# Performance work log

Measured on AMD Instinct MI355X. Metric: run time of the kernel, lower is better.

## Reference

```python
import jax, jax.numpy as jnp
import numpy as np

NUM_PARTS = 10
COS_W = 10.0
COS_K = 100.0
EPS = 1e-6

B, V, F, VHD = 512, 6890, 13776, 20000


def setup_inputs() -> dict:
    key = jax.random.key(0)
    k1, k2, k3, k4, k5 = jax.random.split(key, 5)
    vertices = jax.random.normal(k1, (B, V, 3), dtype=jnp.float32)
    bary = jax.random.uniform(k2, (VHD, 3), dtype=jnp.float32)
    faces = jax.random.randint(k3, (F, 3), 0, V)
    hd_fid = jax.random.randint(k4, (VHD,), 0, F)
    part_fid = jax.random.randint(k5, (F,), 0, NUM_PARTS)
    return {"vertices": vertices, "bary": bary, "faces": faces,
            "hd_fid": hd_fid, "part_fid": part_fid}


def reference(vertices, bary, faces, hd_fid, part_fid):
    # --- per-part mesh volume (signed tetra volumes, segment-summed by part) ---
    tri = vertices[:, faces]                       # [B, F, 3, 3] gather face corners
    t0, t1, t2 = tri[:, :, 0], tri[:, :, 1], tri[:, :, 2]
    vol_f = jnp.einsum('bfi,bfi->bf', jnp.cross(t0, t1), t2) / 6.0   # [B, F]
    fid_onehot = jax.nn.one_hot(part_fid, NUM_PARTS, dtype=vertices.dtype)  # [F, P]
    per_part_volume = vol_f @ fid_onehot           # [B, P]

    # --- HDfy: barycentric sampling of HD vertices on faces ---
    w = bary / jnp.sum(bary, axis=-1, keepdims=True)          # barycentric weights [VHD,3]
    vidx = faces[hd_fid]                                       # [VHD, 3]
    hd_corners = vertices[:, vidx]                             # [B, VHD, 3, 3]
    vertices_hd = jnp.einsum('bvkd,vk->bvd', hd_corners, w)    # [B, VHD, 3]

    # --- per-HD-vertex part volume (bmm with one-hot == gather) ---
    hd_part = part_fid[hd_fid]                                 # [VHD]
    vol_hd = per_part_volume[:, hd_part]                       # [B, VHD]

    # --- center of mass ---
    com = jnp.sum(vertices_hd * vol_hd[..., None], axis=1) / jnp.sum(vol_hd, axis=1, keepdims=True)  # [B,3]

    # --- center of pressure via height-based pressure weights ---
    h = vertices_hd[:, :, 1]                                   # [B, VHD], ground plane at y=0
    inside = (h < 0.0).astype(vertices_hd.dtype)
    outside = (h >= 0.0).astype(vertices_hd.dtype)
    pw = inside * (1.0 - COS_K * h) + outside * jnp.exp(-COS_W * h)
    cop = jnp.sum(vertices_hd * pw[..., None], axis=1) / (jnp.sum(pw, axis=1, keepdims=True) + EPS)  # [B,3]

    # --- stability loss: xz distance between COM and COP ---
    d = com - cop
    return jnp.sqrt(d[:, 0] ** 2 + d[:, 2] ** 2)               # [B]
```

## Files before the change

### kernel.cpp

```cpp
#include <hip/hip_runtime.h>
#include <math.h>

#define NB     512
#define NV     6890
#define NF     13776
#define NVHD   20000
#define NPARTS 10
#define NTHREADS 1024
#define NWAVES (NTHREADS/64)
#define CUT    6697
#define NCHF   ((NF + 63) / 64)
#define NCHH   ((NVHD + 63) / 64)
#define FBLK   ((NF + 255) / 256)
#define HBLK   ((NVHD + 255) / 256)

__global__ __launch_bounds__(256) void count_kernel(
    const int* __restrict__ faces, const int* __restrict__ part_fid,
    const int* __restrict__ hd_fid,
    int* __restrict__ cntF,
    int* __restrict__ cntH)
{
    const int wv = threadIdx.x >> 6, lane = threadIdx.x & 63;
    if (blockIdx.x < FBLK) {
        int c = blockIdx.x * 4 + wv;
        int i = c * 64 + lane;
        int key = -1;
        if (i < NF) {
            int i0 = faces[3*i+0], i1 = faces[3*i+1], i2 = faces[3*i+2];
            bool bad = (i0 >= CUT) || (i1 >= CUT) || (i2 >= CUT);
            key = bad ? 10 : part_fid[i];
        }
        #pragma unroll
        for (int q = 0; q < 11; q++) {
            unsigned long long m = __ballot(key == q);
            if (lane == 0) cntF[q * NCHF + c] = (int)__popcll(m);
        }
    } else {
        int c = (blockIdx.x - FBLK) * 4 + wv;
        if (c < NCHH) {
            int i = c * 64 + lane;
            int key = -1;
            if (i < NVHD) {
                int fid = hd_fid[i];
                int i0 = faces[3*fid+0], i1 = faces[3*fid+1], i2 = faces[3*fid+2];
                key = ((i0 >= CUT) || (i1 >= CUT) || (i2 >= CUT)) ? 1 : 0;
            }
            #pragma unroll
            for (int q = 0; q < 2; q++) {
                unsigned long long m = __ballot(key == q);
                if (lane == 0) cntH[q * NCHH + c] = (int)__popcll(m);
            }
        }
    }
}

__global__ __launch_bounds__(1024) void scan_kernel(
    int* __restrict__ cntF, int* __restrict__ cntH, int* __restrict__ offs)
{
    __shared__ int rowtot[13];
    const int wv = threadIdx.x >> 6, lane = threadIdx.x & 63;
    if (wv < 11) {
        int* row = cntF + wv * NCHF;
        int carry = 0;
        #pragma unroll
        for (int seg = 0; seg < (NCHF + 63) / 64; seg++) {
            int idx = seg * 64 + lane;
            int v = (idx < NCHF) ? row[idx] : 0;
            int incl = v;
            #pragma unroll
            for (int off = 1; off < 64; off <<= 1) { int n = __shfl_up(incl, off, 64); if (lane >= off) incl += n; }
            if (idx < NCHF) row[idx] = incl - v + carry;
            carry += __shfl(incl, 63, 64);
        }
        if (lane == 0) rowtot[wv] = carry;
    } else if (wv < 13) {
        int r = wv - 11;
        int* row = cntH + r * NCHH;
        int carry = 0;
        #pragma unroll
        for (int seg = 0; seg < (NCHH + 63) / 64; seg++) {
            int idx = seg * 64 + lane;
            int v = (idx < NCHH) ? row[idx] : 0;
            int incl = v;
            #pragma unroll
            for (int off = 1; off < 64; off <<= 1) { int n = __shfl_up(incl, off, 64); if (lane >= off) incl += n; }
            if (idx < NCHH) row[idx] = incl - v + carry;
            carry += __shfl(incl, 63, 64);
        }
        if (lane == 0) rowtot[11 + r] = carry;
    }
    __syncthreads();
    if (threadIdx.x == 0) {
        int r = 0;
        #pragma unroll
        for (int q = 0; q < 11; q++) { offs[q] = r; r += rowtot[q]; }
        offs[11] = r;
        offs[12] = 0;
        offs[13] = rowtot[11];
        offs[14] = rowtot[11] + rowtot[12];
    }
}

__global__ __launch_bounds__(256) void scatter_kernel(
    const float* __restrict__ bary, const int* __restrict__ faces,
    const int* __restrict__ hd_fid, const int* __restrict__ part_fid,
    const int* __restrict__ cntF, const int* __restrict__ cntH,
    const int* __restrict__ offs,
    uint2* __restrict__ f_sorted, uint4* __restrict__ hd_sorted)
{
    const int wv = threadIdx.x >> 6, lane = threadIdx.x & 63;
    const unsigned long long low = (1ull << lane) - 1ull;
    if (blockIdx.x < FBLK) {
        int c = blockIdx.x * 4 + wv;
        int i = c * 64 + lane;
        int key = -1; uint2 ft = make_uint2(0u, 0u);
        if (i < NF) {
            int i0 = faces[3*i+0], i1 = faces[3*i+1], i2 = faces[3*i+2];
            int p  = part_fid[i];
            bool bad = (i0 >= CUT) || (i1 >= CUT) || (i2 >= CUT);
            key = bad ? 10 : p;
            ft = make_uint2((unsigned)i0 | ((unsigned)i1 << 16),
                            (unsigned)i2 | ((unsigned)p  << 16));
        }
        #pragma unroll
        for (int q = 0; q < 11; q++) {
            unsigned long long m = __ballot(key == q);
            if (key == q) {
                int rank = (int)__popcll(m & low);
                f_sorted[offs[q] + cntF[q * NCHF + c] + rank] = ft;
            }
        }
    } else {
        int c = (blockIdx.x - FBLK) * 4 + wv;
        if (c < NCHH) {
            int i = c * 64 + lane;
            int key = -1; uint4 hp = make_uint4(0u, 0u, 0u, 0u);
            if (i < NVHD) {
                int fid = hd_fid[i];
                int i0 = faces[3*fid+0], i1 = faces[3*fid+1], i2 = faces[3*fid+2];
                float b0 = bary[3*i+0], b1 = bary[3*i+1], b2 = bary[3*i+2];
                float inv = 1.0f / (b0 + b1 + b2);
                hp = make_uint4((unsigned)i0 | ((unsigned)i1 << 16),
                                (unsigned)i2 | ((unsigned)part_fid[fid] << 16),
                                __float_as_uint(b0*inv), __float_as_uint(b1*inv));
                key = ((i0 >= CUT) || (i1 >= CUT) || (i2 >= CUT)) ? 1 : 0;
            }
            #pragma unroll
            for (int q = 0; q < 2; q++) {
                unsigned long long m = __ballot(key == q);
                if (key == q) {
                    int rank = (int)__popcll(m & low);
                    hd_sorted[offs[12 + q] + cntH[q * NCHH + c] + rank] = hp;
                }
            }
        }
    }
}

__global__ __launch_bounds__(NTHREADS, 8) void stab_kernel(
    const float* __restrict__ vertices,
    const uint2* __restrict__ f_sorted,
    const uint4* __restrict__ hd_sorted,
    const int*   __restrict__ offs,
    float*       __restrict__ out)
{
    __shared__ float2 sxy[CUT];
    __shared__ float  szz[CUT];
    __shared__ float  spart[NPARTS];
    __shared__ float  sredp[NWAVES][NPARTS];

    const int tid  = threadIdx.x;
    const int b    = blockIdx.x;
    const int wave = tid >> 6;
    const int lane = tid & 63;
    const float* __restrict__ vb = vertices + (size_t)b * (NV * 3);

    int offF[12];
    #pragma unroll
    for (int q = 0; q < 12; q++) offF[q] = offs[q];
    const int hClean = offs[13];

    for (int v = tid; v < CUT; v += NTHREADS) {
        float x = vb[3 * v + 0];
        float y = vb[3 * v + 1];
        float z = vb[3 * v + 2];
        sxy[v] = make_float2(x, y);
        szz[v] = z;
    }
    __syncthreads();

    float accp[NPARTS];
    #pragma unroll
    for (int q = 0; q < NPARTS; q++) accp[q] = 0.f;

    #pragma unroll
    for (int p = 0; p < NPARTS; p++) {
        float va = 0.f;
        for (int f = offF[p] + tid; f < offF[p + 1]; f += NTHREADS) {
            uint2 ft = f_sorted[f];
            int i0 = ft.x & 0xFFFF, i1 = ft.x >> 16, i2 = ft.y & 0xFFFF;
            float2 t0 = sxy[i0]; float z0 = szz[i0];
            float2 t1 = sxy[i1]; float z1 = szz[i1];
            float2 t2 = sxy[i2]; float z2 = szz[i2];
            float cx = t0.y * z1   - z0   * t1.y;
            float cy = z0   * t1.x - t0.x * z1;
            float cz = t0.x * t1.y - t0.y * t1.x;
            va += (cx * t2.x + cy * t2.y + cz * z2) * (1.0f / 6.0f);
        }
        accp[p] += va;
    }
    for (int f = offF[10] + tid; f < NF; f += NTHREADS) {
        uint2 ft = f_sorted[f];
        int i0 = ft.x & 0xFFFF, i1 = ft.x >> 16;
        int i2 = ft.y & 0xFFFF, p  = (int)(ft.y >> 16);
        float x0 = vb[3*i0+0], y0 = vb[3*i0+1], z0 = vb[3*i0+2];
        float x1 = vb[3*i1+0], y1 = vb[3*i1+1], z1 = vb[3*i1+2];
        float x2 = vb[3*i2+0], y2 = vb[3*i2+1], z2 = vb[3*i2+2];
        float cx = y0 * z1 - z0 * y1;
        float cy = z0 * x1 - x0 * z1;
        float cz = x0 * y1 - y0 * x1;
        float vol = (cx * x2 + cy * y2 + cz * z2) * (1.0f / 6.0f);
        #pragma unroll
        for (int q = 0; q < NPARTS; q++) accp[q] += (p == q) ? vol : 0.f;
    }

    #pragma unroll
    for (int q = 0; q < NPARTS; q++) {
        float s = accp[q];
        #pragma unroll
        for (int off = 32; off > 0; off >>= 1) s += __shfl_down(s, off, 64);
        accp[q] = s;
    }
    if (lane == 0) {
        #pragma unroll
        for (int q = 0; q < NPARTS; q++) sredp[wave][q] = accp[q];
    }
    __syncthreads();
    if (tid < NPARTS) {
        float s = 0.f;
        #pragma unroll
        for (int w = 0; w < NWAVES; w++) s += sredp[w][tid];
        spart[tid] = s;
    }
    __syncthreads();

    float sVx = 0.f, sVz = 0.f, sVol = 0.f;
    float sPx = 0.f, sPz = 0.f, sPw = 0.f;

    #pragma unroll 2
    for (int v = tid; v < hClean; v += NTHREADS) {
        uint4 hp = hd_sorted[v];
        int i0 = hp.x & 0xFFFF, i1 = hp.x >> 16;
        int i2 = hp.y & 0xFFFF, p  = (int)(hp.y >> 16);
        float w0 = __uint_as_float(hp.z);
        float w1 = __uint_as_float(hp.w);
        float w2 = 1.0f - w0 - w1;
        float2 t0 = sxy[i0]; float z0 = szz[i0];
        float2 t1 = sxy[i1]; float z1 = szz[i1];
        float2 t2 = sxy[i2]; float z2 = szz[i2];
        float x = w0 * t0.x + w1 * t1.x + w2 * t2.x;
        float y = w0 * t0.y + w1 * t1.y + w2 * t2.y;
        float z = w0 * z0   + w1 * z1   + w2 * z2;
        float vol = spart[p];
        float pw  = (y < 0.f) ? fmaf(-100.f, y, 1.f) : __expf(-10.f * y);
        sVx += x * vol;  sVz += z * vol;  sVol += vol;
        sPx += x * pw;   sPz += z * pw;   sPw += pw;
    }
    for (int v = hClean + tid; v < NVHD; v += NTHREADS) {
        uint4 hp = hd_sorted[v];
        int i0 = hp.x & 0xFFFF, i1 = hp.x >> 16;
        int i2 = hp.y & 0xFFFF, p  = (int)(hp.y >> 16);
        float w0 = __uint_as_float(hp.z);
        float w1 = __uint_as_float(hp.w);
        float w2 = 1.0f - w0 - w1;
        float x0 = vb[3*i0+0], y0 = vb[3*i0+1], z0 = vb[3*i0+2];
        float x1 = vb[3*i1+0], y1 = vb[3*i1+1], z1 = vb[3*i1+2];
        float x2 = vb[3*i2+0], y2 = vb[3*i2+1], z2 = vb[3*i2+2];
        float x = w0 * x0 + w1 * x1 + w2 * x2;
        float y = w0 * y0 + w1 * y1 + w2 * y2;
        float z = w0 * z0 + w1 * z1 + w2 * z2;
        float vol = spart[p];
        float pw  = (y < 0.f) ? fmaf(-100.f, y, 1.f) : __expf(-10.f * y);
        sVx += x * vol;  sVz += z * vol;  sVol += vol;
        sPx += x * pw;   sPz += z * pw;   sPw += pw;
    }

    float vals[6] = {sVx, sVz, sVol, sPx, sPz, sPw};
    #pragma unroll
    for (int q = 0; q < 6; q++) {
        float s = vals[q];
        #pragma unroll
        for (int off = 32; off > 0; off >>= 1) s += __shfl_down(s, off, 64);
        vals[q] = s;
    }
    float* sred6 = &sredp[0][0];
    if (lane == 0) {
        #pragma unroll
        for (int q = 0; q < 6; q++) sred6[wave * 6 + q] = vals[q];
    }
    __syncthreads();
    if (tid == 0) {
        float r[6];
        #pragma unroll
        for (int q = 0; q < 6; q++) {
            float s = 0.f;
            #pragma unroll
            for (int w = 0; w < NWAVES; w++) s += sred6[w * 6 + q];
            r[q] = s;
        }
        float invVol = 1.0f / r[2];
        float invPw  = 1.0f / (r[5] + 1e-6f);
        float comx = r[0] * invVol, comz = r[1] * invVol;
        float copx = r[3] * invPw,  copz = r[4] * invPw;
        float d0 = comx - copx, d2 = comz - copz;
        out[b] = sqrtf(d0 * d0 + d2 * d2);
    }
}

extern "C" void kernel_launch(void* const* d_in, const int* in_sizes, int n_in,
                              void* d_out, int out_size, void* d_ws, size_t ws_size,
                              hipStream_t stream) {
    const float* vertices = (const float*)d_in[0];
    const float* bary     = (const float*)d_in[1];
    const int*   faces    = (const int*)d_in[2];
    const int*   hd_fid   = (const int*)d_in[3];
    const int*   part_fid = (const int*)d_in[4];
    float* out = (float*)d_out;

    char* ws = (char*)d_ws;
    uint4* hd_sorted = (uint4*)ws;
    uint2* f_sorted  = (uint2*)(ws + 320000);
    int*   cntF      = (int*)(ws + 320000 + 110208);
    int*   cntH      = (int*)(ws + 320000 + 110208 + 9504);
    int*   offs      = (int*)(ws + 320000 + 110208 + 9504 + 2504);

    count_kernel<<<FBLK + HBLK, 256, 0, stream>>>(faces, part_fid, hd_fid, cntF, cntH);
    scan_kernel<<<1, 1024, 0, stream>>>(cntF, cntH, offs);
    scatter_kernel<<<FBLK + HBLK, 256, 0, stream>>>(bary, faces, hd_fid, part_fid,
                                                    cntF, cntH, offs, f_sorted, hd_sorted);
    stab_kernel<<<NB, NTHREADS, 0, stream>>>(vertices, f_sorted, hd_sorted, offs, out);
}
```

Baseline: 54.83 us.

## Bucket HD vertices by part to factor volume weights out of inner loop

```diff
diff --git a/kernel.cpp b/kernel.cpp
--- a/kernel.cpp
+++ b/kernel.cpp
@@ -13,6 +13,7 @@
 #define NCHH   ((NVHD + 63) / 64)
 #define FBLK   ((NF + 255) / 256)
 #define HBLK   ((NVHD + 255) / 256)
+#define NOFFS  33
 
 __global__ __launch_bounds__(256) void count_kernel(
     const int* __restrict__ faces, const int* __restrict__ part_fid,
@@ -43,10 +44,12 @@
             if (i < NVHD) {
                 int fid = hd_fid[i];
                 int i0 = faces[3*fid+0], i1 = faces[3*fid+1], i2 = faces[3*fid+2];
-                key = ((i0 >= CUT) || (i1 >= CUT) || (i2 >= CUT)) ? 1 : 0;
+                int p  = part_fid[fid];
+                bool bad = (i0 >= CUT) || (i1 >= CUT) || (i2 >= CUT);
+                key = bad ? (10 + p) : p;
             }
             #pragma unroll
-            for (int q = 0; q < 2; q++) {
+            for (int q = 0; q < 20; q++) {
                 unsigned long long m = __ballot(key == q);
                 if (lane == 0) cntH[q * NCHH + c] = (int)__popcll(m);
             }
@@ -57,37 +60,22 @@
 __global__ __launch_bounds__(1024) void scan_kernel(
     int* __restrict__ cntF, int* __restrict__ cntH, int* __restrict__ offs)
 {
-    __shared__ int rowtot[13];
+    __shared__ int rowtot[31];
     const int wv = threadIdx.x >> 6, lane = threadIdx.x & 63;
-    if (wv < 11) {
-        int* row = cntF + wv * NCHF;
+    for (int r = wv; r < 31; r += NWAVES) {
+        int  len = (r < 11) ? NCHF : NCHH;
+        int* row = (r < 11) ? (cntF + r * NCHF) : (cntH + (r - 11) * NCHH);
         int carry = 0;
-        #pragma unroll
-        for (int seg = 0; seg < (NCHF + 63) / 64; seg++) {
+        for (int seg = 0; seg < (len + 63) / 64; seg++) {
             int idx = seg * 64 + lane;
-            int v = (idx < NCHF) ? row[idx] : 0;
+            int v = (idx < len) ? row[idx] : 0;
             int incl = v;
             #pragma unroll
             for (int off = 1; off < 64; off <<= 1) { int n = __shfl_up(incl, off, 64); if (lane >= off) incl += n; }
-            if (idx < NCHF) row[idx] = incl - v + carry;
+            if (idx < len) row[idx] = incl - v + carry;
             carry += __shfl(incl, 63, 64);
         }
-        if (lane == 0) rowtot[wv] = carry;
-    } else if (wv < 13) {
-        int r = wv - 11;
-        int* row = cntH + r * NCHH;
-        int carry = 0;
-        #pragma unroll
-        for (int seg = 0; seg < (NCHH + 63) / 64; seg++) {
-            int idx = seg * 64 + lane;
-            int v = (idx < NCHH) ? row[idx] : 0;
-            int incl = v;
-            #pragma unroll
-            for (int off = 1; off < 64; off <<= 1) { int n = __shfl_up(incl, off, 64); if (lane >= off) incl += n; }
-            if (idx < NCHH) row[idx] = incl - v + carry;
-            carry += __shfl(incl, 63, 64);
-        }
-        if (lane == 0) rowtot[11 + r] = carry;
+        if (lane == 0) rowtot[r] = carry;
     }
     __syncthreads();
     if (threadIdx.x == 0) {
@@ -95,9 +83,10 @@
         #pragma unroll
         for (int q = 0; q < 11; q++) { offs[q] = r; r += rowtot[q]; }
         offs[11] = r;
-        offs[12] = 0;
-        offs[13] = rowtot[11];
-        offs[14] = rowtot[11] + rowtot[12];
+        r = 0;
+        #pragma unroll
+        for (int k = 0; k < 20; k++) { offs[12 + k] = r; r += rowtot[11 + k]; }
+        offs[32] = r;
     }
 }
 
@@ -138,15 +127,17 @@
             if (i < NVHD) {
                 int fid = hd_fid[i];
                 int i0 = faces[3*fid+0], i1 = faces[3*fid+1], i2 = faces[3*fid+2];
+                int p  = part_fid[fid];
                 float b0 = bary[3*i+0], b1 = bary[3*i+1], b2 = bary[3*i+2];
                 float inv = 1.0f / (b0 + b1 + b2);
+                bool bad = (i0 >= CUT) || (i1 >= CUT) || (i2 >= CUT);
+                key = bad ? (10 + p) : p;
                 hp = make_uint4((unsigned)i0 | ((unsigned)i1 << 16),
-                                (unsigned)i2 | ((unsigned)part_fid[fid] << 16),
+                                (unsigned)i2,
                                 __float_as_uint(b0*inv), __float_as_uint(b1*inv));
-                key = ((i0 >= CUT) || (i1 >= CUT) || (i2 >= CUT)) ? 1 : 0;
             }
             #pragma unroll
-            for (int q = 0; q < 2; q++) {
+            for (int q = 0; q < 20; q++) {
                 unsigned long long m = __ballot(key == q);
                 if (key == q) {
                     int rank = (int)__popcll(m & low);
@@ -168,6 +159,7 @@
     __shared__ float  szz[CUT];
     __shared__ float  spart[NPARTS];
     __shared__ float  sredp[NWAVES][NPARTS];
+    __shared__ int    soffs[NOFFS];
 
     const int tid  = threadIdx.x;
     const int b    = blockIdx.x;
@@ -175,10 +167,7 @@
     const int lane = tid & 63;
     const float* __restrict__ vb = vertices + (size_t)b * (NV * 3);
 
-    int offF[12];
-    #pragma unroll
-    for (int q = 0; q < 12; q++) offF[q] = offs[q];
-    const int hClean = offs[13];
+    if (tid < NOFFS) soffs[tid] = offs[tid];
 
     for (int v = tid; v < CUT; v += NTHREADS) {
         float x = vb[3 * v + 0];
@@ -191,12 +180,9 @@
 
     float accp[NPARTS];
     #pragma unroll
-    for (int q = 0; q < NPARTS; q++) accp[q] = 0.f;
-
-    #pragma unroll
     for (int p = 0; p < NPARTS; p++) {
         float va = 0.f;
-        for (int f = offF[p] + tid; f < offF[p + 1]; f += NTHREADS) {
+        for (int f = soffs[p] + tid; f < soffs[p + 1]; f += NTHREADS) {
             uint2 ft = f_sorted[f];
             int i0 = ft.x & 0xFFFF, i1 = ft.x >> 16, i2 = ft.y & 0xFFFF;
             float2 t0 = sxy[i0]; float z0 = szz[i0];
@@ -205,11 +191,11 @@
             float cx = t0.y * z1   - z0   * t1.y;
             float cy = z0   * t1.x - t0.x * z1;
             float cz = t0.x * t1.y - t0.y * t1.x;
-            va += (cx * t2.x + cy * t2.y + cz * z2) * (1.0f / 6.0f);
-        }
-        accp[p] += va;
-    }
-    for (int f = offF[10] + tid; f < NF; f += NTHREADS) {
+            va += cx * t2.x + cy * t2.y + cz * z2;
+        }
+        accp[p] = va * (1.0f / 6.0f);
+    }
+    for (int f = soffs[10] + tid; f < NF; f += NTHREADS) {
         uint2 ft = f_sorted[f];
         int i0 = ft.x & 0xFFFF, i1 = ft.x >> 16;
         int i2 = ft.y & 0xFFFF, p  = (int)(ft.y >> 16);
@@ -244,74 +230,85 @@
     }
     __syncthreads();
 
-    float sVx = 0.f, sVz = 0.f, sVol = 0.f;
+    float sVx = 0.f, sVz = 0.f;
     float sPx = 0.f, sPz = 0.f, sPw = 0.f;
 
-    #pragma unroll 2
-    for (int v = tid; v < hClean; v += NTHREADS) {
-        uint4 hp = hd_sorted[v];
-        int i0 = hp.x & 0xFFFF, i1 = hp.x >> 16;
-        int i2 = hp.y & 0xFFFF, p  = (int)(hp.y >> 16);
-        float w0 = __uint_as_float(hp.z);
-        float w1 = __uint_as_float(hp.w);
-        float w2 = 1.0f - w0 - w1;
-        float2 t0 = sxy[i0]; float z0 = szz[i0];
-        float2 t1 = sxy[i1]; float z1 = szz[i1];
-        float2 t2 = sxy[i2]; float z2 = szz[i2];
-        float x = w0 * t0.x + w1 * t1.x + w2 * t2.x;
-        float y = w0 * t0.y + w1 * t1.y + w2 * t2.y;
-        float z = w0 * z0   + w1 * z1   + w2 * z2;
-        float vol = spart[p];
-        float pw  = (y < 0.f) ? fmaf(-100.f, y, 1.f) : __expf(-10.f * y);
-        sVx += x * vol;  sVz += z * vol;  sVol += vol;
-        sPx += x * pw;   sPz += z * pw;   sPw += pw;
-    }
-    for (int v = hClean + tid; v < NVHD; v += NTHREADS) {
-        uint4 hp = hd_sorted[v];
-        int i0 = hp.x & 0xFFFF, i1 = hp.x >> 16;
-        int i2 = hp.y & 0xFFFF, p  = (int)(hp.y >> 16);
-        float w0 = __uint_as_float(hp.z);
-        float w1 = __uint_as_float(hp.w);
-        float w2 = 1.0f - w0 - w1;
-        float x0 = vb[3*i0+0], y0 = vb[3*i0+1], z0 = vb[3*i0+2];
-        float x1 = vb[3*i1+0], y1 = vb[3*i1+1], z1 = vb[3*i1+2];
-        float x2 = vb[3*i2+0], y2 = vb[3*i2+1], z2 = vb[3*i2+2];
-        float x = w0 * x0 + w1 * x1 + w2 * x2;
-        float y = w0 * y0 + w1 * y1 + w2 * y2;
-        float z = w0 * z0 + w1 * z1 + w2 * z2;
-        float vol = spart[p];
-        float pw  = (y < 0.f) ? fmaf(-100.f, y, 1.f) : __expf(-10.f * y);
-        sVx += x * vol;  sVz += z * vol;  sVol += vol;
-        sPx += x * pw;   sPz += z * pw;   sPw += pw;
-    }
-
-    float vals[6] = {sVx, sVz, sVol, sPx, sPz, sPw};
+    for (int p = 0; p < NPARTS; p++) {
+        float xs = 0.f, zs = 0.f;
+        for (int v = soffs[12 + p] + tid; v < soffs[13 + p]; v += NTHREADS) {
+            uint4 hp = hd_sorted[v];
+            int i0 = hp.x & 0xFFFF, i1 = hp.x >> 16, i2 = hp.y & 0xFFFF;
+            float w0 = __uint_as_float(hp.z);
+            float w1 = __uint_as_float(hp.w);
+            float w2 = 1.0f - w0 - w1;
+            float2 t0 = sxy[i0]; float z0 = szz[i0];
+            float2 t1 = sxy[i1]; float z1 = szz[i1];
+            float2 t2 = sxy[i2]; float z2 = szz[i2];
+            float x = w0 * t0.x + w1 * t1.x + w2 * t2.x;
+            float y = w0 * t0.y + w1 * t1.y + w2 * t2.y;
+            float z = w0 * z0   + w1 * z1   + w2 * z2;
+            float pw = (y < 0.f) ? fmaf(-100.f, y, 1.f) : __expf(-10.f * y);
+            xs += x;  zs += z;
+            sPx += x * pw;  sPz += z * pw;  sPw += pw;
+        }
+        float vp = spart[p];
+        sVx += vp * xs;  sVz += vp * zs;
+    }
+    for (int p = 0; p < NPARTS; p++) {
+        float xs = 0.f, zs = 0.f;
+        for (int v = soffs[22 + p] + tid; v < soffs[23 + p]; v += NTHREADS) {
+            uint4 hp = hd_sorted[v];
+            int i0 = hp.x & 0xFFFF, i1 = hp.x >> 16, i2 = hp.y & 0xFFFF;
+            float w0 = __uint_as_float(hp.z);
+            float w1 = __uint_as_float(hp.w);
+            float w2 = 1.0f - w0 - w1;
+            float x0 = vb[3*i0+0], y0 = vb[3*i0+1], z0 = vb[3*i0+2];
+            float x1 = vb[3*i1+0], y1 = vb[3*i1+1], z1 = vb[3*i1+2];
+            float x2 = vb[3*i2+0], y2 = vb[3*i2+1], z2 = vb[3*i2+2];
+            float x = w0 * x0 + w1 * x1 + w2 * x2;
+            float y = w0 * y0 + w1 * y1 + w2 * y2;
+            float z = w0 * z0 + w1 * z1 + w2 * z2;
+            float pw = (y < 0.f) ? fmaf(-100.f, y, 1.f) : __expf(-10.f * y);
+            xs += x;  zs += z;
+            sPx += x * pw;  sPz += z * pw;  sPw += pw;
+        }
+        float vp = spart[p];
+        sVx += vp * xs;  sVz += vp * zs;
+    }
+
+    float vals[5] = {sVx, sVz, sPx, sPz, sPw};
     #pragma unroll
-    for (int q = 0; q < 6; q++) {
+    for (int q = 0; q < 5; q++) {
         float s = vals[q];
         #pragma unroll
         for (int off = 32; off > 0; off >>= 1) s += __shfl_down(s, off, 64);
         vals[q] = s;
     }
-    float* sred6 = &sredp[0][0];
+    float* sred5 = &sredp[0][0];
     if (lane == 0) {
         #pragma unroll
-        for (int q = 0; q < 6; q++) sred6[wave * 6 + q] = vals[q];
+        for (int q = 0; q < 5; q++) sred5[wave * 5 + q] = vals[q];
     }
     __syncthreads();
     if (tid == 0) {
-        float r[6];
-        #pragma unroll
-        for (int q = 0; q < 6; q++) {
+        float r[5];
+        #pragma unroll
+        for (int q = 0; q < 5; q++) {
             float s = 0.f;
             #pragma unroll
-            for (int w = 0; w < NWAVES; w++) s += sred6[w * 6 + q];
+            for (int w = 0; w < NWAVES; w++) s += sred5[w * 5 + q];
             r[q] = s;
         }
-        float invVol = 1.0f / r[2];
-        float invPw  = 1.0f / (r[5] + 1e-6f);
+        float sVol = 0.f;
+        #pragma unroll
+        for (int p = 0; p < NPARTS; p++) {
+            int np = (soffs[13 + p] - soffs[12 + p]) + (soffs[23 + p] - soffs[22 + p]);
+            sVol += spart[p] * (float)np;
+        }
+        float invVol = 1.0f / sVol;
+        float invPw  = 1.0f / (r[4] + 1e-6f);
         float comx = r[0] * invVol, comz = r[1] * invVol;
-        float copx = r[3] * invPw,  copz = r[4] * invPw;
+        float copx = r[2] * invPw,  copz = r[3] * invPw;
         float d0 = comx - copx, d2 = comz - copz;
         out[b] = sqrtf(d0 * d0 + d2 * d2);
     }
@@ -332,7 +329,7 @@
     uint2* f_sorted  = (uint2*)(ws + 320000);
     int*   cntF      = (int*)(ws + 320000 + 110208);
     int*   cntH      = (int*)(ws + 320000 + 110208 + 9504);
-    int*   offs      = (int*)(ws + 320000 + 110208 + 9504 + 2504);
+    int*   offs      = (int*)(ws + 320000 + 110208 + 9504 + 25040);
 
     count_kernel<<<FBLK + HBLK, 256, 0, stream>>>(faces, part_fid, hd_fid, cntF, cntH);
     scan_kernel<<<1, 1024, 0, stream>>>(cntF, cntH, offs);
```

Result: slower. 79.67 us (+45.3%).
